# Optimization experiments

Measured on AMD Instinct MI355X. Metric: run time of the kernel, lower is better.

The kernel has to match this reference:

```python
import jax, jax.numpy as jnp
import numpy as np

B, V, DIM, HEADS = 8192, 17, 192, 3
DKH = DIM // HEADS


def setup_inputs() -> dict:
    key = jax.random.key(0)
    ks = jax.random.split(key, 10)
    s = DIM ** -0.5
    return {
        "x": jax.random.normal(ks[0], (B, V, DIM), jnp.float32),
        "mask": jax.random.uniform(ks[1], (V, V), jnp.float32),
        "group_mask": jax.random.normal(ks[2], (B, HEADS, V, V), jnp.float32),
        "drop_mask": jax.random.bernoulli(ks[3], 0.5, (B, HEADS, V)).astype(jnp.float32),
        "qkv_w": jax.random.normal(ks[4], (3 * DIM, DIM), jnp.float32) * s,  # 1x1 conv == linear
        "qkv_b": jnp.zeros((3 * DIM,), jnp.float32),
        "attn_w": jax.random.normal(ks[5], (DIM, DIM), jnp.float32) * s,
        "attn_b": jnp.zeros((DIM,), jnp.float32),
        "key_rel": jax.random.normal(ks[6], (V * V - V, DKH), jnp.float32),
        "key_rel_diag": jax.random.normal(ks[7], (1, DKH), jnp.float32),
        "PA": jnp.ones((V, V), jnp.float32),
        "nn1_w": jax.random.normal(ks[8], (DIM, DIM), jnp.float32) * s,
        "nn1_b": jnp.zeros((DIM,), jnp.float32),
    }


def _forward(x, mask, group_mask, drop_mask, qkv_w, qkv_b, attn_w, attn_b,
             key_rel, key_rel_diag, PA, nn1_w, nn1_b):
    Bsz, Vn, C = x.shape
    Nh = HEADS
    dkh = C // Nh
    # 1x1 qkv conv over the channel axis (T=1 singleton time axis drops out)
    qkv = x @ qkv_w.T + qkv_b                      # (B, V, 3C)
    q, k, v = qkv[..., :C], qkv[..., C:2 * C], qkv[..., 2 * C:]

    def heads(t):
        return t.reshape(Bsz, Vn, Nh, dkh).transpose(0, 2, 1, 3)  # (B, Nh, V, dkh)

    q = heads(q) * (dkh ** -0.5)
    k = heads(k)
    v = heads(v)

    logits = jnp.einsum('bhid,bhjd->bhij', q, k)   # (B, Nh, V, V)
    logits = logits + (mask * PA)[None, None] + group_mask

    # relative position logits (rel_to_abs gather trick)
    rel = jnp.einsum('bhid,ijd->bhij', q, key_rel.reshape(Vn, Vn - 1, dkh))  # (B,Nh,V,V-1)
    diag = jnp.einsum('bhid,d->bhi', q, key_rel_diag[0])                     # (B,Nh,V)
    r = rel.reshape(Bsz, Nh, Vn - 1, Vn)           # reinterpret flat (V*(V-1)) as (V-1, V)
    r = jnp.concatenate([r, jnp.zeros((Bsz, Nh, 1, Vn), r.dtype)], axis=2)   # pad row -> (B,Nh,V,V)
    r = jnp.concatenate([diag[..., None], r], axis=3)                        # diag col -> (B,Nh,V,V+1)
    rel_logits = r.reshape(Bsz, Nh, Vn + 1, Vn)[:, :, :Vn, :]                # (B,Nh,V,V)

    w = jax.nn.softmax(logits + rel_logits, axis=-1)
    # stochastic column (key) mask + renormalize
    w = w * drop_mask[:, :, None, :]
    w = w / (w.sum(-1, keepdims=True) + 1e-8)

    out = jnp.einsum('bhij,bhjd->bhid', w, v)      # (B, Nh, V, dkh)
    out = out.transpose(0, 2, 1, 3).reshape(Bsz, Vn, C)  # combine heads (channel = h*dkh+d)
    out = out @ attn_w.T + attn_b                  # 1x1 attn_out conv
    out = out @ nn1_w.T + nn1_b                    # nn1 linear (dropout in eval -> identity)
    return out


def reference(x, mask, group_mask, drop_mask, qkv_w, qkv_b, attn_w, attn_b,
              key_rel, key_rel_diag, PA, nn1_w, nn1_b):
    return _forward(x, mask, group_mask, drop_mask, qkv_w, qkv_b, attn_w, attn_b,
                    key_rel, key_rel_diag, PA, nn1_w, nn1_b)
```

## Files before the change

kernel.cpp:

```cpp
#include <hip/hip_runtime.h>

typedef __attribute__((ext_vector_type(8))) short short8;
typedef __attribute__((ext_vector_type(4))) float f32x4;
typedef __attribute__((ext_vector_type(16))) float f32x16;
typedef unsigned short u16;
typedef unsigned int u32;

#define NB_TOT 8192
#define DIM 192

#define WN_OFF    0
#define WCN_OFF   221184
#define BC_OFF    294912
#define KRELF_OFF 295680
#define MPA_OFF   365312

#define XS_O 0
#define KV_O 9600
#define Q_O  24288
#define DR_O 33888
#define SMEM_U16 34092

__device__ __forceinline__ u16 f2b(float f) {
  u32 u = __float_as_uint(f);
  u32 r = u + 0x7FFFu + ((u >> 16) & 1u);
  return (u16)(r >> 16);
}

__device__ __forceinline__ void bar_lgkm() {
  asm volatile("s_waitcnt lgkmcnt(0)" ::: "memory");
  __builtin_amdgcn_s_barrier();
  asm volatile("" ::: "memory");
}

__global__ void prep_kernel(const float* __restrict__ qkv_w,
                            const float* __restrict__ attn_w,
                            const float* __restrict__ attn_b,
                            const float* __restrict__ nn1_w,
                            const float* __restrict__ nn1_b,
                            const float* __restrict__ key_rel,
                            const float* __restrict__ krd,
                            const float* __restrict__ mask,
                            const float* __restrict__ PA,
                            char* __restrict__ ws) {
  u16* wN    = (u16*)(ws + WN_OFF);
  u16* wcN   = (u16*)(ws + WCN_OFF);
  float* bc  = (float*)(ws + BC_OFF);
  u16* krelf = (u16*)(ws + KRELF_OFF);
  float* mpa = (float*)(ws + MPA_OFF);
  for (int idx = blockIdx.x * 256 + threadIdx.x; idx < 152289; idx += gridDim.x * 256) {
    if (idx < 110592) {
      wN[idx] = f2b(qkv_w[idx]);
    } else if (idx < 147456) {
      int t2 = idx - 110592; int n = t2 / 192, k = t2 - n * 192;
      float a = 0.f;
      for (int t = 0; t < 192; ++t) a = fmaf(nn1_w[n * 192 + t], attn_w[t * 192 + k], a);
      wcN[n * 192 + k] = f2b(a);
    } else if (idx < 147648) {
      int n = idx - 147456; float a = nn1_b[n];
      for (int t = 0; t < 192; ++t) a = fmaf(nn1_w[n * 192 + t], attn_b[t], a);
      bc[n] = a;
    } else if (idx < 152000) {
      int t = idx - 147648;
      int lane = t & 63, ks = (t >> 6) & 3, I = t >> 8;
      int J = lane & 31;
      int d0 = ks * 16 + (lane >> 5) * 8;
      u16 vals[8];
#pragma unroll
      for (int i = 0; i < 8; ++i) {
        float v = 0.f;
        if (J <= 16) {
          if (J == I) v = krd[d0 + i];
          else { int tt = 17 * I + J; int p = tt - tt / 18 - 1; v = key_rel[p * 64 + d0 + i]; }
        }
        vals[i] = f2b(v);
      }
      u32 w0 = vals[0] | ((u32)vals[1] << 16), w1 = vals[2] | ((u32)vals[3] << 16);
      u32 w2 = vals[4] | ((u32)vals[5] << 16), w3 = vals[6] | ((u32)vals[7] << 16);
      uint4 pk; pk.x = w0; pk.y = w1; pk.z = w2; pk.w = w3;
      *(uint4*)(krelf + (size_t)t * 8) = pk;
    } else {
      int i = idx - 152000; mpa[i] = mask[i] * PA[i];
    }
  }
}

__global__ __launch_bounds__(512, 2)
void fused_kernel(const float* __restrict__ x, const float* __restrict__ gm,
                  const float* __restrict__ drop, const float* __restrict__ qkv_b,
                  const u16* __restrict__ wN, const u16* __restrict__ wcN,
                  const float* __restrict__ bc, const u16* __restrict__ krelf,
                  const float* __restrict__ mpa, float* __restrict__ out) {
  __shared__ u16 smem[SMEM_U16];
  float* const Sf    = (float*)(smem + XS_O);
  u16*   const wbf   = smem + XS_O + 3672;
  float* const dropl = (float*)(smem + DR_O);

  const int tid = threadIdx.x;
  const int blk = blockIdx.x;

  float gmr[4];
  const float* gmb = gm + (size_t)blk * 1734;
#pragma unroll
  for (int it = 0; it < 4; ++it) {
    int e = tid + it * 512;
    gmr[it] = (e < 1734) ? gmb[e] : 0.f;
  }

  const float* xb = x + (size_t)blk * 34 * 192;
  for (int idx = tid; idx < 2304; idx += 512) {
    int row = idx / 48, k4 = (idx - row * 48) * 4;
    uint2 pk;
    if (row < 34) {
      float4 v = *(const float4*)(xb + row * 192 + k4);
      u16 p[4] = {f2b(v.x), f2b(v.y), f2b(v.z), f2b(v.w)};
      pk = *(uint2*)p;
    } else { pk.x = 0; pk.y = 0; }
    *(uint2*)(smem + XS_O + row * 200 + k4) = pk;
  }
  if (tid < 102) dropl[tid] = drop[(size_t)blk * 102 + tid];
  bar_lgkm();

  const int lrow = tid & 15, lg = (tid >> 4) & 3, kgrp = lg * 8;
  const int wv = tid >> 6;

  for (int N = wv; N < 36; N += 8) {
    const int c0 = N * 16;
    const int which = c0 / 192;
    const int hd = c0 - which * 192;
    const int h = hd >> 6;
    const int d = (hd & 63) + lrow;
    const int c = c0 + lrow;
    const u16* wB = wN + (size_t)c * 192;
    short8 bfr[6];
#pragma unroll
    for (int kk = 0; kk < 6; ++kk)
      bfr[kk] = *(const short8*)(wB + kk * 32 + kgrp);
    const float bias = qkv_b[c];
    const float scale = which ? 1.0f : 0.125f;
    const int sb = (which == 0) ? Q_O : (which == 1) ? KV_O : (KV_O + 7344);
#pragma unroll
    for (int m = 0; m < 3; ++m) {
      f32x4 acc = {};
#pragma unroll
      for (int kk = 0; kk < 6; ++kk) {
        short8 a = *(const short8*)(smem + XS_O + (m * 16 + lrow) * 200 + kk * 32 + kgrp);
        acc = __builtin_amdgcn_mfma_f32_16x16x32_bf16(a, bfr[kk], acc, 0, 0, 0);
      }
#pragma unroll
      for (int j = 0; j < 4; ++j) {
        int r = m * 16 + lg * 4 + j;
        if (r < 34) {
          int bi = r >= 17 ? 1 : 0, I = r - bi * 17;
          smem[sb + (bi * 3 + h) * 1224 + I * 72 + d] = f2b((acc[j] + bias) * scale);
        }
      }
    }
  }
  bar_lgkm();

#pragma unroll
  for (int it = 0; it < 4; ++it) {
    int e = tid + it * 512;
    if (e < 1734) {
      int bi = e / 867, rem = e - bi * 867;
      int h = rem / 289, r2 = rem - h * 289;
      int I = r2 / 17, J = r2 - I * 17;
      Sf[((bi * 3 + h) * 17 + I) * 18 + J] = gmr[it] + mpa[r2];
    }
  }
  bar_lgkm();

  const int lane = tid & 63;
  const int l31 = lane & 31;
  const int lh = lane >> 5;
  const int rowc = l31 < 16 ? l31 : 16;

  if (wv < 6) {
    int bh = wv;
    int bi = bh >= 3 ? 1 : 0, h = bh - bi * 3;
    const u16* qb = smem + Q_O + (bi * 3 + h) * 1224 + rowc * 72;
    const u16* kb = smem + KV_O + (bi * 3 + h) * 1224 + rowc * 72;
    f32x16 acc = {};
#pragma unroll
    for (int ks = 0; ks < 4; ++ks) {
      short8 afr = *(const short8*)(qb + ks * 16 + lh * 8);
      short8 bfr = *(const short8*)(kb + ks * 16 + lh * 8);
      acc = __builtin_amdgcn_mfma_f32_32x32x16_bf16(afr, bfr, acc, 0, 0, 0);
    }
    if (l31 < 17) {
      float* Sb = Sf + (bh * 17) * 18 + l31;
#pragma unroll
      for (int g = 0; g < 16; ++g) {
        int I = (g & 3) + 8 * (g >> 2) + 4 * lh;
        if (I < 17) Sb[I * 18] += acc[g];
      }
    }
  }
  bar_lgkm();

  for (int I = wv; I < 17; I += 8) {
    int bhA = l31 < 6 ? l31 : 5;
    int biA = bhA >= 3 ? 1 : 0, hA = bhA - biA * 3;
    const u16* qb = smem + Q_O + (biA * 3 + hA) * 1224 + I * 72;
    f32x16 acc = {};
#pragma unroll
    for (int ks = 0; ks < 4; ++ks) {
      short8 afr = *(const short8*)(qb + ks * 16 + lh * 8);
      short8 bfr = *(const short8*)(krelf + ((size_t)(I * 4 + ks) * 64 + lane) * 8);
      acc = __builtin_amdgcn_mfma_f32_32x32x16_bf16(afr, bfr, acc, 0, 0, 0);
    }
    if (l31 < 17) {
#pragma unroll
      for (int g = 0; g < 16; ++g) {
        int bh = (g & 3) + 8 * (g >> 2) + 4 * lh;
        if (bh < 6) Sf[(bh * 17 + I) * 18 + l31] += acc[g];
      }
    }
  }
  bar_lgkm();

  if (tid < 102) {
    int bh = tid / 17, I = tid - bh * 17;
    float* row = Sf + (bh * 17 + I) * 18;
    float lv[17];
#pragma unroll
    for (int J = 0; J < 17; ++J) lv[J] = row[J];
    float m = lv[0];
#pragma unroll
    for (int J = 1; J < 17; ++J) m = fmaxf(m, lv[J]);
    float s1 = 0.f;
#pragma unroll
    for (int J = 0; J < 17; ++J) { lv[J] = __expf(lv[J] - m); s1 += lv[J]; }
    const float* dr = dropl + bh * 17;
    float inv1 = 1.0f / s1, s2 = 0.f;
#pragma unroll
    for (int J = 0; J < 17; ++J) { float w2 = lv[J] * inv1 * dr[J]; lv[J] = w2; s2 += w2; }
    float inv2 = 1.0f / (s2 + 1e-8f);
    u32* wr32 = (u32*)(wbf + (bh * 17 + I) * 32);
    int sw = (I & 3) << 2;
#pragma unroll
    for (int k2 = 0; k2 < 16; ++k2) {
      u16 lo = (2 * k2 < 17) ? f2b(lv[2 * k2] * inv2) : (u16)0;
      u16 hi = (2 * k2 + 1 < 17) ? f2b(lv[2 * k2 + 1] * inv2) : (u16)0;
      wr32[k2 ^ sw] = lo | ((u32)hi << 16);
    }
  }
  bar_lgkm();

  if (wv < 6) {
    int bh = wv;
    const u16* wb = wbf + (bh * 17 + rowc) * 32;
    int sw = (rowc & 3) << 3;
    short8 wa0 = *(const short8*)(wb + ((lh * 8) ^ sw));
    short8 wa1 = *(const short8*)(wb + ((lh * 8 + 16) ^ sw));
    int bi = bh >= 3 ? 1 : 0, h = bh - bi * 3;
    const u16* vb = smem + KV_O + 7344 + (bi * 3 + h) * 1224;
    f32x16 acc[2] = {{}, {}};
#pragma unroll
    for (int nt = 0; nt < 2; ++nt) {
      int d = nt * 32 + l31;
      short8 v0;
#pragma unroll
      for (int i = 0; i < 8; ++i) v0[i] = (short)vb[(lh * 8 + i) * 72 + d];
      acc[nt] = __builtin_amdgcn_mfma_f32_32x32x16_bf16(wa0, v0, acc[nt], 0, 0, 0);
      short8 v1 = {};
      if (lh == 0) v1[0] = (short)vb[16 * 72 + d];
      acc[nt] = __builtin_amdgcn_mfma_f32_32x32x16_bf16(wa1, v1, acc[nt], 0, 0, 0);
    }
#pragma unroll
    for (int nt = 0; nt < 2; ++nt) {
      int d = nt * 32 + l31;
#pragma unroll
      for (int g = 0; g < 16; ++g) {
        int I = (g & 3) + 8 * (g >> 2) + 4 * lh;
        if (I < 17) smem[Q_O + (bi * 17 + I) * 200 + h * 64 + d] = f2b(acc[nt][g]);
      }
    }
  }
  bar_lgkm();

  float* outb = out + (size_t)blk * 34 * 192;
  for (int n = wv; n < 12; n += 8) {
    const int nc = n * 16 + lrow;
    short8 bfr[6];
#pragma unroll
    for (int kk = 0; kk < 6; ++kk)
      bfr[kk] = *(const short8*)(wcN + (size_t)nc * 192 + kk * 32 + kgrp);
    const float bias = bc[nc];
#pragma unroll
    for (int m = 0; m < 3; ++m) {
      f32x4 acc = {};
#pragma unroll
      for (int kk = 0; kk < 6; ++kk) {
        short8 a = *(const short8*)(smem + Q_O + (m * 16 + lrow) * 200 + kk * 32 + kgrp);
        acc = __builtin_amdgcn_mfma_f32_16x16x32_bf16(a, bfr[kk], acc, 0, 0, 0);
      }
#pragma unroll
      for (int j = 0; j < 4; ++j) {
        int r = m * 16 + lg * 4 + j;
        if (r < 34) outb[(size_t)r * 192 + nc] = acc[j] + bias;
      }
    }
  }
}

extern "C" void kernel_launch(void* const* d_in, const int* in_sizes, int n_in,
                              void* d_out, int out_size, void* d_ws, size_t ws_size,
                              hipStream_t stream) {
  const float* x    = (const float*)d_in[0];
  const float* mask = (const float*)d_in[1];
  const float* gm   = (const float*)d_in[2];
  const float* drop = (const float*)d_in[3];
  const float* qkvw = (const float*)d_in[4];
  const float* qkvb = (const float*)d_in[5];
  const float* attw = (const float*)d_in[6];
  const float* attb = (const float*)d_in[7];
  const float* krel = (const float*)d_in[8];
  const float* krd  = (const float*)d_in[9];
  const float* PA   = (const float*)d_in[10];
  const float* nn1w = (const float*)d_in[11];
  const float* nn1b = (const float*)d_in[12];
  char* ws = (char*)d_ws;
  float* out = (float*)d_out;

  prep_kernel<<<600, 256, 0, stream>>>(qkvw, attw, attb, nn1w, nn1b, krel, krd, mask, PA, ws);

  const u16* wN    = (const u16*)(ws + WN_OFF);
  const u16* wcN   = (const u16*)(ws + WCN_OFF);
  const float* bc  = (const float*)(ws + BC_OFF);
  const u16* krelf = (const u16*)(ws + KRELF_OFF);
  const float* mpa = (const float*)(ws + MPA_OFF);

  fused_kernel<<<NB_TOT / 2, 512, 0, stream>>>(x, gm, drop, qkvb, wN, wcN, bc, krelf, mpa, out);
}
```

Measured before the change: 194.5 us.

## Compact and XOR-swizzle LDS layout for Q/K/V, raise launch bounds occupancy hint

```diff
diff --git a/kernel.cpp b/kernel.cpp
--- a/kernel.cpp
+++ b/kernel.cpp
@@ -16,10 +16,11 @@
 #define MPA_OFF   365312
 
 #define XS_O 0
-#define KV_O 9600
-#define Q_O  24288
-#define DR_O 33888
-#define SMEM_U16 34092
+#define K_O  7072
+#define V_O  13600
+#define Q_O  20128
+#define DR_O 26752
+#define SMEM_U16 26956
 
 __device__ __forceinline__ u16 f2b(float f) {
   u32 u = __float_as_uint(f);
@@ -85,7 +86,7 @@
   }
 }
 
-__global__ __launch_bounds__(512, 2)
+__global__ __launch_bounds__(512, 6)
 void fused_kernel(const float* __restrict__ x, const float* __restrict__ gm,
                   const float* __restrict__ drop, const float* __restrict__ qkv_b,
                   const u16* __restrict__ wN, const u16* __restrict__ wcN,
@@ -93,7 +94,7 @@
                   const float* __restrict__ mpa, float* __restrict__ out) {
   __shared__ u16 smem[SMEM_U16];
   float* const Sf    = (float*)(smem + XS_O);
-  u16*   const wbf   = smem + XS_O + 3672;
+  u16*   const wbf   = smem + K_O;
   float* const dropl = (float*)(smem + DR_O);
 
   const int tid = threadIdx.x;
@@ -108,15 +109,11 @@
   }
 
   const float* xb = x + (size_t)blk * 34 * 192;
-  for (int idx = tid; idx < 2304; idx += 512) {
+  for (int idx = tid; idx < 1632; idx += 512) {
     int row = idx / 48, k4 = (idx - row * 48) * 4;
-    uint2 pk;
-    if (row < 34) {
-      float4 v = *(const float4*)(xb + row * 192 + k4);
-      u16 p[4] = {f2b(v.x), f2b(v.y), f2b(v.z), f2b(v.w)};
-      pk = *(uint2*)p;
-    } else { pk.x = 0; pk.y = 0; }
-    *(uint2*)(smem + XS_O + row * 200 + k4) = pk;
+    float4 v = *(const float4*)(xb + row * 192 + k4);
+    u16 p[4] = {f2b(v.x), f2b(v.y), f2b(v.z), f2b(v.w)};
+    *(uint2*)(smem + XS_O + row * 208 + k4) = *(uint2*)p;
   }
   if (tid < 102) dropl[tid] = drop[(size_t)blk * 102 + tid];
   bar_lgkm();
@@ -138,13 +135,12 @@
       bfr[kk] = *(const short8*)(wB + kk * 32 + kgrp);
     const float bias = qkv_b[c];
     const float scale = which ? 1.0f : 0.125f;
-    const int sb = (which == 0) ? Q_O : (which == 1) ? KV_O : (KV_O + 7344);
 #pragma unroll
     for (int m = 0; m < 3; ++m) {
       f32x4 acc = {};
 #pragma unroll
       for (int kk = 0; kk < 6; ++kk) {
-        short8 a = *(const short8*)(smem + XS_O + (m * 16 + lrow) * 200 + kk * 32 + kgrp);
+        short8 a = *(const short8*)(smem + XS_O + (m * 16 + lrow) * 208 + kk * 32 + kgrp);
         acc = __builtin_amdgcn_mfma_f32_16x16x32_bf16(a, bfr[kk], acc, 0, 0, 0);
       }
 #pragma unroll
@@ -152,7 +148,11 @@
         int r = m * 16 + lg * 4 + j;
         if (r < 34) {
           int bi = r >= 17 ? 1 : 0, I = r - bi * 17;
-          smem[sb + (bi * 3 + h) * 1224 + I * 72 + d] = f2b((acc[j] + bias) * scale);
+          int slot = bi * 3 + h;
+          u16 val = f2b((acc[j] + bias) * scale);
+          if (which == 0)      smem[Q_O + slot * 1104 + I * 64 + (d ^ ((I & 7) << 3))] = val;
+          else if (which == 1) smem[K_O + slot * 1088 + I * 64 + (d ^ ((I & 7) << 3))] = val;
+          else                 smem[V_O + slot * 1088 + I * 64 + d] = val;
         }
       }
     }
@@ -165,8 +165,7 @@
     if (e < 1734) {
       int bi = e / 867, rem = e - bi * 867;
       int h = rem / 289, r2 = rem - h * 289;
-      int I = r2 / 17, J = r2 - I * 17;
-      Sf[((bi * 3 + h) * 17 + I) * 18 + J] = gmr[it] + mpa[r2];
+      Sf[(bi * 3 + h) * 289 + r2] = gmr[it] + mpa[r2];
     }
   }
   bar_lgkm();
@@ -178,22 +177,23 @@
 
   if (wv < 6) {
     int bh = wv;
-    int bi = bh >= 3 ? 1 : 0, h = bh - bi * 3;
-    const u16* qb = smem + Q_O + (bi * 3 + h) * 1224 + rowc * 72;
-    const u16* kb = smem + KV_O + (bi * 3 + h) * 1224 + rowc * 72;
+    const u16* qb = smem + Q_O + bh * 1104;
+    const u16* kb = smem + K_O + bh * 1088;
+    const int swr = (rowc & 7) << 3;
     f32x16 acc = {};
 #pragma unroll
     for (int ks = 0; ks < 4; ++ks) {
-      short8 afr = *(const short8*)(qb + ks * 16 + lh * 8);
-      short8 bfr = *(const short8*)(kb + ks * 16 + lh * 8);
+      int off = (ks * 16 + lh * 8) ^ swr;
+      short8 afr = *(const short8*)(qb + rowc * 64 + off);
+      short8 bfr = *(const short8*)(kb + rowc * 64 + off);
       acc = __builtin_amdgcn_mfma_f32_32x32x16_bf16(afr, bfr, acc, 0, 0, 0);
     }
     if (l31 < 17) {
-      float* Sb = Sf + (bh * 17) * 18 + l31;
+      float* Sb = Sf + bh * 289 + l31;
 #pragma unroll
       for (int g = 0; g < 16; ++g) {
         int I = (g & 3) + 8 * (g >> 2) + 4 * lh;
-        if (I < 17) Sb[I * 18] += acc[g];
+        if (I < 17) Sb[I * 17] += acc[g];
       }
     }
   }
@@ -201,12 +201,12 @@
 
   for (int I = wv; I < 17; I += 8) {
     int bhA = l31 < 6 ? l31 : 5;
-    int biA = bhA >= 3 ? 1 : 0, hA = bhA - biA * 3;
-    const u16* qb = smem + Q_O + (biA * 3 + hA) * 1224 + I * 72;
+    const u16* qb = smem + Q_O + bhA * 1104 + I * 64;
+    const int swz = (I & 7) << 3;
     f32x16 acc = {};
 #pragma unroll
     for (int ks = 0; ks < 4; ++ks) {
-      short8 afr = *(const short8*)(qb + ks * 16 + lh * 8);
+      short8 afr = *(const short8*)(qb + ((ks * 16 + lh * 8) ^ swz));
       short8 bfr = *(const short8*)(krelf + ((size_t)(I * 4 + ks) * 64 + lane) * 8);
       acc = __builtin_amdgcn_mfma_f32_32x32x16_bf16(afr, bfr, acc, 0, 0, 0);
     }
@@ -214,7 +214,7 @@
 #pragma unroll
       for (int g = 0; g < 16; ++g) {
         int bh = (g & 3) + 8 * (g >> 2) + 4 * lh;
-        if (bh < 6) Sf[(bh * 17 + I) * 18 + l31] += acc[g];
+        if (bh < 6) Sf[bh * 289 + I * 17 + l31] += acc[g];
       }
     }
   }
@@ -222,7 +222,7 @@
 
   if (tid < 102) {
     int bh = tid / 17, I = tid - bh * 17;
-    float* row = Sf + (bh * 17 + I) * 18;
+    float* row = Sf + bh * 289 + I * 17;
     float lv[17];
 #pragma unroll
     for (int J = 0; J < 17; ++J) lv[J] = row[J];
@@ -255,17 +255,17 @@
     short8 wa0 = *(const short8*)(wb + ((lh * 8) ^ sw));
     short8 wa1 = *(const short8*)(wb + ((lh * 8 + 16) ^ sw));
     int bi = bh >= 3 ? 1 : 0, h = bh - bi * 3;
-    const u16* vb = smem + KV_O + 7344 + (bi * 3 + h) * 1224;
+    const u16* vb = smem + V_O + bh * 1088;
     f32x16 acc[2] = {{}, {}};
 #pragma unroll
     for (int nt = 0; nt < 2; ++nt) {
       int d = nt * 32 + l31;
       short8 v0;
 #pragma unroll
-      for (int i = 0; i < 8; ++i) v0[i] = (short)vb[(lh * 8 + i) * 72 + d];
+      for (int i = 0; i < 8; ++i) v0[i] = (short)vb[(lh * 8 + i) * 64 + d];
       acc[nt] = __builtin_amdgcn_mfma_f32_32x32x16_bf16(wa0, v0, acc[nt], 0, 0, 0);
       short8 v1 = {};
-      if (lh == 0) v1[0] = (short)vb[16 * 72 + d];
+      if (lh == 0) v1[0] = (short)vb[16 * 64 + d];
       acc[nt] = __builtin_amdgcn_mfma_f32_32x32x16_bf16(wa1, v1, acc[nt], 0, 0, 0);
     }
 #pragma unroll
@@ -274,7 +274,7 @@
 #pragma unroll
       for (int g = 0; g < 16; ++g) {
         int I = (g & 3) + 8 * (g >> 2) + 4 * lh;
-        if (I < 17) smem[Q_O + (bi * 17 + I) * 200 + h * 64 + d] = f2b(acc[nt][g]);
+        if (I < 17) smem[XS_O + (bi * 17 + I) * 208 + h * 64 + d] = f2b(acc[nt][g]);
       }
     }
   }
@@ -293,7 +293,7 @@
       f32x4 acc = {};
 #pragma unroll
       for (int kk = 0; kk < 6; ++kk) {
-        short8 a = *(const short8*)(smem + Q_O + (m * 16 + lrow) * 200 + kk * 32 + kgrp);
+        short8 a = *(const short8*)(smem + XS_O + (m * 16 + lrow) * 208 + kk * 32 + kgrp);
         acc = __builtin_amdgcn_mfma_f32_16x16x32_bf16(a, bfr[kk], acc, 0, 0, 0);
       }
 #pragma unroll
```

Result: slower. 262.1 us (+34.7%).
